# Kernel tuning notes

Measured on AMD Instinct MI355X. Metric: run time of the kernel, lower is better.

Reference implementation:

```python
import jax, jax.numpy as jnp
import numpy as np

N_ATOMS = 5000
N_EDGES = 100000
F = 128          # num_features
B = 20           # num_basis (sinc expansion)
L = 3            # num_interactions
CUTOFF = 5.0
NUM_EMB = 119


def setup_inputs() -> dict:
    key = jax.random.key(0)
    ks = jax.random.split(key, 16)
    Z = jax.random.randint(ks[0], (N_ATOMS,), 1, NUM_EMB)
    edge_idx = jax.random.randint(ks[1], (N_EDGES, 2), 0, N_ATOMS)
    edge_dist = jax.random.uniform(ks[2], (N_EDGES,), minval=0.5, maxval=6.0, dtype=jnp.float32)
    u = jax.random.normal(ks[3], (N_EDGES, 3), dtype=jnp.float32)
    u = u / jnp.linalg.norm(u, axis=-1, keepdims=True)
    edge_diff = u * edge_dist[:, None]  # displacement vectors with |d| == edge_dist
    s = lambda k, shape: (jax.random.normal(k, shape, dtype=jnp.float32) * 0.05)
    inp = dict(Z=Z, edge_idx=edge_idx, edge_diff=edge_diff, edge_dist=edge_dist)
    inp.update(
        emb=s(ks[4], (NUM_EMB, F)),
        msg_w1=s(ks[5], (L, F, F)), msg_b1=jnp.zeros((L, F), jnp.float32),
        msg_w2=s(ks[6], (L, F, 3 * F)), msg_b2=jnp.zeros((L, 3 * F), jnp.float32),
        filt_w=s(ks[7], (L, B, 3 * F)), filt_b=jnp.zeros((L, 3 * F), jnp.float32),
        upd_U=s(ks[8], (L, F, F)), upd_V=s(ks[9], (L, F, F)),
        upd_w1=s(ks[10], (L, 2 * F, F)), upd_b1=jnp.zeros((L, F), jnp.float32),
        upd_w2=s(ks[11], (L, F, 3 * F)), upd_b2=jnp.zeros((L, 3 * F), jnp.float32),
        ro_w1=s(ks[12], (F, F // 2)), ro_b1=jnp.zeros((F // 2,), jnp.float32),
        ro_w2=s(ks[13], (F // 2, 1)), ro_b2=jnp.zeros((1,), jnp.float32),
    )
    return inp


def _painn(Z, edge_idx, edge_diff, edge_dist,
           emb, msg_w1, msg_b1, msg_w2, msg_b2, filt_w, filt_b,
           upd_U, upd_V, upd_w1, upd_b1, upd_w2, upd_b2,
           ro_w1, ro_b1, ro_w2, ro_b2):
    dtype = edge_diff.dtype
    # edge mask (equivalent to boolean compaction: masked edges contribute 0)
    mask = (edge_dist < CUTOFF).astype(dtype)
    dst = edge_idx[:, 0]  # receiver (index_add target)
    src = edge_idx[:, 1]  # sender (gathered neighbor)
    # sinc radial expansion: sin(n*pi*r/rc)/r, n = 1..B
    n = jnp.arange(1, B + 1, dtype=dtype)
    rbf = jnp.sin(edge_dist[:, None] * n * (jnp.pi / CUTOFF)) / edge_dist[:, None]  # [E,B]
    # cosine cutoff envelope, zeroed outside cutoff
    fc = 0.5 * (jnp.cos(jnp.pi * edge_dist / CUTOFF) + 1.0)
    env = (fc * mask)[:, None]  # [E,1]
    unit = edge_diff / edge_dist[:, None]  # [E,3]

    s_feat = emb[Z]                                   # [N,F]
    v_feat = jnp.zeros((Z.shape[0], 3, F), dtype)     # [N,3,F]

    for l in range(L):
        # ---- PainnMessage ----
        filt = (rbf @ filt_w[l] + filt_b[l]) * env                           # [E,3F]
        phi = jax.nn.silu(s_feat @ msg_w1[l] + msg_b1[l]) @ msg_w2[l] + msg_b2[l]  # [N,3F]
        fo = filt * phi[src]                                                  # [E,3F]
        gsv, gev, ms = jnp.split(fo, 3, axis=-1)                              # each [E,F]
        mv = v_feat[src] * gsv[:, None, :] + gev[:, None, :] * unit[:, :, None]  # [E,3,F]
        s_feat = s_feat + jnp.zeros_like(s_feat).at[dst].add(ms)
        v_feat = v_feat + jnp.zeros_like(v_feat).at[dst].add(mv)
        # ---- PainnUpdate ----
        Uv = jnp.einsum('nif,fg->nig', v_feat, upd_U[l])   # [N,3,F]
        Vv = jnp.einsum('nif,fg->nig', v_feat, upd_V[l])   # [N,3,F]
        Vn = jnp.linalg.norm(Vv, axis=1)                   # [N,F]
        a = jax.nn.silu(jnp.concatenate([s_feat, Vn], axis=-1) @ upd_w1[l] + upd_b1[l]) @ upd_w2[l] + upd_b2[l]
        avv, asv, ass = jnp.split(a, 3, axis=-1)
        v_feat = v_feat + avv[:, None, :] * Uv
        s_feat = s_feat + asv * jnp.sum(Uv * Vv, axis=1) + ass

    # atomwise readout MLP -> per-atom energy
    atom_energy = (jax.nn.silu(s_feat @ ro_w1 + ro_b1) @ ro_w2 + ro_b2)[:, 0]  # [N]
    return atom_energy


def reference(Z, edge_idx, edge_diff, edge_dist,
              emb, msg_w1, msg_b1, msg_w2, msg_b2, filt_w, filt_b,
              upd_U, upd_V, upd_w1, upd_b1, upd_w2, upd_b2,
              ro_w1, ro_b1, ro_w2, ro_b2):
    return _painn(Z, edge_idx, edge_diff, edge_dist,
                  emb, msg_w1, msg_b1, msg_w2, msg_b2, filt_w, filt_b,
                  upd_U, upd_V, upd_w1, upd_b1, upd_w2, upd_b2,
                  ro_w1, ro_b1, ro_w2, ro_b2)
```

## Files before the change

kernel.cpp:

```cpp
#include <hip/hip_runtime.h>
#include <hip/hip_bf16.h>
#include <hip/hip_fp16.h>
#include <math.h>

#define N_ATOMS 5000
#define N_EDGES 100000
#define F 128
#define B 20
#define NL 3
#define CAP 64

constexpr float CUTOFF = 5.0f;
constexpr float PI_F = 3.14159265358979323846f;

typedef _Float16 f16x8 __attribute__((ext_vector_type(8)));
typedef _Float16 h2 __attribute__((ext_vector_type(2)));
typedef float f32x4 __attribute__((ext_vector_type(4)));

struct EMeta { int src; float env; float u0, u1, u2; int pad[3]; };
struct __align__(4) U3 { unsigned int x, y, z; };

__device__ __forceinline__ float silu_f(float x) { return x / (1.0f + __expf(-x)); }

#define PV_IDX(atom, t) (((size_t)(atom) * F + (t)) * 6)

__global__ void init_kernel(const int* __restrict__ Z, const float* __restrict__ emb,
                            float* __restrict__ s, _Float16* __restrict__ s_h,
                            float* __restrict__ v, _Float16* __restrict__ pv,
                            int* __restrict__ count) {
    int atom = blockIdx.x;
    int t = threadIdx.x;
    float val = emb[Z[atom] * F + t];
    s[atom * F + t] = val;
    s_h[atom * F + t] = (_Float16)val;
#pragma unroll
    for (int d = 0; d < 3; ++d) v[(size_t)atom * 3 * F + d * F + t] = 0.0f;
    unsigned int* pp = (unsigned int*)(pv + PV_IDX(atom, t));
    pp[0] = 0u; pp[1] = 0u; pp[2] = 0u;
    if (t == 0) count[atom] = 0;
}

__global__ void fill_buckets(const int* __restrict__ eidx, int* __restrict__ count,
                             int* __restrict__ bucket) {
    int e = blockIdx.x * 256 + threadIdx.x;
    if (e >= N_EDGES) return;
    int dst = eidx[2 * e];
    int pos = atomicAdd(&count[dst], 1);
    if (pos < CAP) bucket[dst * CAP + pos] = e;
}

__global__ void edge_meta_kernel(const int* __restrict__ count, const int* __restrict__ bucket,
                                 const int* __restrict__ eidx, const float* __restrict__ ediff,
                                 const float* __restrict__ edist,
                                 EMeta* __restrict__ meta, _Float16* __restrict__ rbfh) {
    int slot = blockIdx.x * 256 + threadIdx.x;
    if (slot >= N_ATOMS * CAP) return;
    int a = slot / CAP, i = slot % CAP;
    if (i >= count[a]) return;
    int e = bucket[slot];
    float d = edist[e];
    EMeta m;
    m.src = eidx[2 * e + 1];
    float fc = 0.5f * (cosf(PI_F * d / CUTOFF) + 1.0f);
    m.env = (d < CUTOFF) ? fc : 0.0f;
    float inv = 1.0f / d;
    m.u0 = ediff[3 * e + 0] * inv;
    m.u1 = ediff[3 * e + 1] * inv;
    m.u2 = ediff[3 * e + 2] * inv;
    m.pad[0] = m.pad[1] = m.pad[2] = 0;
    meta[slot] = m;
    _Float16* rp = rbfh + (size_t)slot * 24;
#pragma unroll
    for (int b = 0; b < B; ++b)
        rp[b] = (_Float16)(sinf(d * (float)(b + 1) * (PI_F / CUTOFF)) / d);
    rp[20] = rp[21] = rp[22] = rp[23] = (_Float16)0.0f;
}

struct TPlanX { const float* src; void* dst; int R, C, blk0, isf16, pad; };
struct TPlansX { TPlanX p[24]; int n; };

__global__ void transpose_x(TPlansX P) {
    int b = blockIdx.x;
    int pi = 0;
#pragma unroll
    for (int i = 1; i < 24; ++i)
        if (i < P.n && b >= P.p[i].blk0) pi = i;
    const float* src = P.p[pi].src;
    int R = P.p[pi].R, C = P.p[pi].C, pad = P.p[pi].pad;
    int f = (b - P.p[pi].blk0) * 256 + threadIdx.x;
    if (f < R * C) {
        int c = f / R, r = f - c * R;
        float val = src[r * C + c];
        if (P.p[pi].isf16) ((_Float16*)P.p[pi].dst)[c * pad + r] = (_Float16)val;
        else ((float*)P.p[pi].dst)[c * pad + r] = val;
    }
}

__global__ __launch_bounds__(256) void phi_mlp_kernel(
    const _Float16* __restrict__ s_h, const _Float16* __restrict__ w1T,
    const float* __restrict__ b1, const _Float16* __restrict__ w2T,
    const float* __restrict__ b2, _Float16* __restrict__ pv) {
    __shared__ __align__(16) _Float16 shA[16 * 136];
    __shared__ __align__(16) _Float16 shH[16 * 136];
    int r0 = blockIdx.x * 16;
    int tid = threadIdx.x;
    {
        int r = tid >> 4, c8 = (tid & 15) * 8;
        int rg = r0 + r; if (rg >= N_ATOMS) rg = N_ATOMS - 1;
        *(f16x8*)(shA + r * 136 + c8) = *(const f16x8*)(s_h + (size_t)rg * F + c8);
    }
    __syncthreads();
    int lane = tid & 63, wv = tid >> 6;
    int col = lane & 15, quad = lane >> 4;
    for (int nt = wv; nt < 8; nt += 4) {
        int n = nt * 16 + col;
        f32x4 acc = {0.f, 0.f, 0.f, 0.f};
#pragma unroll
        for (int kt = 0; kt < 4; ++kt) {
            f16x8 afr = *(const f16x8*)(shA + col * 136 + kt * 32 + quad * 8);
            f16x8 bfr = *(const f16x8*)(w1T + (size_t)n * 128 + kt * 32 + quad * 8);
            acc = __builtin_amdgcn_mfma_f32_16x16x32_f16(afr, bfr, acc, 0, 0, 0);
        }
        float bb = b1[n];
#pragma unroll
        for (int r = 0; r < 4; ++r)
            shH[(quad * 4 + r) * 136 + n] = (_Float16)silu_f(acc[r] + bb);
    }
    __syncthreads();
    for (int nt = wv; nt < 24; nt += 4) {
        int n = nt * 16 + col;
        f32x4 acc = {0.f, 0.f, 0.f, 0.f};
#pragma unroll
        for (int kt = 0; kt < 4; ++kt) {
            f16x8 afr = *(const f16x8*)(shH + col * 136 + kt * 32 + quad * 8);
            f16x8 bfr = *(const f16x8*)(w2T + (size_t)n * 128 + kt * 32 + quad * 8);
            acc = __builtin_amdgcn_mfma_f32_16x16x32_f16(afr, bfr, acc, 0, 0, 0);
        }
        float bb = b2[n];
#pragma unroll
        for (int r = 0; r < 4; ++r) {
            int row = r0 + quad * 4 + r;
            if (row < N_ATOMS)
                pv[PV_IDX(row, n & 127) + (n >> 7)] = (_Float16)(acc[r] + bb);
        }
    }
}

__global__ __launch_bounds__(256) void edge_agg_kernel(
    const int* __restrict__ count, const EMeta* __restrict__ meta,
    const _Float16* __restrict__ rbfh,
    const _Float16* __restrict__ fwT,
    const float* __restrict__ fb,
    const _Float16* __restrict__ pv,
    float* __restrict__ s, float* __restrict__ v,
    _Float16* __restrict__ vmid_h) {
    int a = blockIdx.x;
    int tid = threadIdx.x;
    int t = tid & 127;
    int team = tid >> 7;

    unsigned int rw0[10], rw1[10], rw2[10];
    {
        const unsigned int* p0 = (const unsigned int*)(fwT + (size_t)t * 24);
        const unsigned int* p1 = (const unsigned int*)(fwT + (size_t)(F + t) * 24);
        const unsigned int* p2 = (const unsigned int*)(fwT + (size_t)(2 * F + t) * 24);
#pragma unroll
        for (int j = 0; j < 10; ++j) { rw0[j] = p0[j]; rw1[j] = p1[j]; rw2[j] = p2[j]; }
    }
    float fb0 = fb[t], fb1 = fb[F + t], fb2 = fb[2 * F + t];

    int n = count[a]; if (n > CAP) n = CAP;
    float accS = 0.f, accV0 = 0.f, accV1 = 0.f, accV2 = 0.f;

    __shared__ int sh_src[32];
    __shared__ float sh_env[32];
    __shared__ float sh_unit[32][3];
    __shared__ __align__(16) unsigned int sh_rbf[32 * 12];
    __shared__ __align__(16) float sh_part[4][F];
    const size_t aC = (size_t)a * CAP;
    const unsigned int* rbf32 = (const unsigned int*)rbfh;

    for (int base = 0; base < n; base += 32) {
        int cnt = min(32, n - base);
        __syncthreads();
        if (tid < cnt) {
            EMeta m = meta[aC + base + tid];
            sh_src[tid] = m.src;
            sh_env[tid] = m.env;
            sh_unit[tid][0] = m.u0; sh_unit[tid][1] = m.u1; sh_unit[tid][2] = m.u2;
        }
        for (int task = tid; task < cnt * 12; task += 256) {
            int i = task / 12, w = task - i * 12;
            sh_rbf[i * 12 + w] = rbf32[(aC + base + i) * 12 + w];
        }
        __syncthreads();

        int myCnt = (cnt > team) ? ((cnt - team + 1) >> 1) : 0;
        if (myCnt > 0) {
            U3 QA[4], QB[4];
            int ngrp = (myCnt + 3) >> 2;

            auto load_grp = [&](int gbase, U3 Q[4]) {
#pragma unroll
                for (int j = 0; j < 4; ++j) {
                    int i = gbase + j;
                    int ii = (i < myCnt) ? i : (myCnt - 1);
                    int src = sh_src[team + 2 * ii];
                    Q[j] = *(const U3*)(pv + PV_IDX(src, t));
                }
            };
            auto comp_grp = [&](int gbase, U3 Q[4]) {
#pragma unroll
                for (int j = 0; j < 4; ++j) {
                    int i = gbase + j;
                    if (i < myCnt) {
                        int ei = team + 2 * i;
                        const uint4* rq = (const uint4*)(sh_rbf + ei * 12);
                        uint4 qa = rq[0], qb = rq[1];
                        uint2 qc = *(const uint2*)(sh_rbf + ei * 12 + 8);
                        unsigned int rr[10] = {qa.x, qa.y, qa.z, qa.w,
                                               qb.x, qb.y, qb.z, qb.w, qc.x, qc.y};
                        float f0 = fb0, f1 = fb1, f2 = fb2;
#pragma unroll
                        for (int p = 0; p < 10; ++p) {
                            h2 rb = __builtin_bit_cast(h2, rr[p]);
                            f0 = __builtin_amdgcn_fdot2(rb, __builtin_bit_cast(h2, rw0[p]), f0, false);
                            f1 = __builtin_amdgcn_fdot2(rb, __builtin_bit_cast(h2, rw1[p]), f1, false);
                            f2 = __builtin_amdgcn_fdot2(rb, __builtin_bit_cast(h2, rw2[p]), f2, false);
                        }
                        float env = sh_env[ei];
                        f0 *= env; f1 *= env; f2 *= env;
                        h2 q0 = __builtin_bit_cast(h2, Q[j].x);
                        h2 q1 = __builtin_bit_cast(h2, Q[j].y);
                        h2 q2 = __builtin_bit_cast(h2, Q[j].z);
                        accS += f2 * (float)q1[0];
                        float gsv = f0 * (float)q0[0];
                        float gev = f1 * (float)q0[1];
                        accV0 += (float)q1[1] * gsv + gev * sh_unit[ei][0];
                        accV1 += (float)q2[0] * gsv + gev * sh_unit[ei][1];
                        accV2 += (float)q2[1] * gsv + gev * sh_unit[ei][2];
                    }
                }
            };

            load_grp(0, QA);
            for (int g = 0; g < ngrp; g += 2) {
                if (g + 1 < ngrp) load_grp((g + 1) * 4, QB);
                comp_grp(g * 4, QA);
                if (g + 1 < ngrp) {
                    if (g + 2 < ngrp) load_grp((g + 2) * 4, QA);
                    comp_grp((g + 1) * 4, QB);
                }
            }
        }
    }

    __syncthreads();
    if (team == 1) {
        sh_part[0][t] = accS; sh_part[1][t] = accV0;
        sh_part[2][t] = accV1; sh_part[3][t] = accV2;
    }
    __syncthreads();
    if (team == 0) {
        float sm = s[a * F + t] + accS + sh_part[0][t];
        s[a * F + t] = sm;
        float vm0 = v[a * 3 * F + t] + accV0 + sh_part[1][t];
        float vm1 = v[a * 3 * F + F + t] + accV1 + sh_part[2][t];
        float vm2 = v[a * 3 * F + 2 * F + t] + accV2 + sh_part[3][t];
        v[a * 3 * F + t] = vm0;
        v[a * 3 * F + F + t] = vm1;
        v[a * 3 * F + 2 * F + t] = vm2;
        vmid_h[(size_t)(a * 3 + 0) * F + t] = (_Float16)vm0;
        vmid_h[(size_t)(a * 3 + 1) * F + t] = (_Float16)vm1;
        vmid_h[(size_t)(a * 3 + 2) * F + t] = (_Float16)vm2;
    }
}

__global__ __launch_bounds__(512) void fused_update_kernel(
    const _Float16* __restrict__ vmid_h, const _Float16* __restrict__ uvT,
    const _Float16* __restrict__ w1T, const float* __restrict__ b1,
    const _Float16* __restrict__ w2T, const float* __restrict__ b2,
    float* __restrict__ s, float* __restrict__ v, _Float16* __restrict__ pv,
    const _Float16* __restrict__ nw1T, const float* __restrict__ nb1,
    const _Float16* __restrict__ nw2T, const float* __restrict__ nb2,
    int do_phi,
    const _Float16* __restrict__ roT16, const float* __restrict__ rb1,
    const float* __restrict__ rw2, const float* __restrict__ rb2,
    float* __restrict__ out, int do_ro) {
    __shared__ __align__(16) _Float16 shA[48 * 136];
    __shared__ __align__(16) _Float16 shUV[48 * 264];
    __shared__ __align__(16) _Float16 shCat[16 * 264];
    __shared__ __align__(16) _Float16 shH[16 * 136];
    __shared__ __align__(16) _Float16 shAa[16 * 392];
    _Float16* shS = shA;
    float* shRO = (float*)shAa;
    int a0 = blockIdx.x * 16;
    int r0 = a0 * 3;
    int tid = threadIdx.x;
    for (int slot = tid; slot < 48 * 16; slot += 512) {
        int r = slot >> 4, c8 = (slot & 15) * 8;
        int rg = r0 + r; if (rg >= N_ATOMS * 3) rg = N_ATOMS * 3 - 1;
        *(f16x8*)(shA + r * 136 + c8) = *(const f16x8*)(vmid_h + (size_t)rg * F + c8);
    }
    __syncthreads();
    int lane = tid & 63, wv = tid >> 6;
    int col = lane & 15, quad = lane >> 4;

    for (int j = wv; j < 48; j += 8) {
        int mt = j >> 4, nt = j & 15;
        int n = nt * 16 + col;
        f32x4 acc = {0.f, 0.f, 0.f, 0.f};
#pragma unroll
        for (int kt = 0; kt < 4; ++kt) {
            f16x8 afr = *(const f16x8*)(shA + (mt * 16 + col) * 136 + kt * 32 + quad * 8);
            f16x8 bfr = *(const f16x8*)(uvT + (size_t)n * 128 + kt * 32 + quad * 8);
            acc = __builtin_amdgcn_mfma_f32_16x16x32_f16(afr, bfr, acc, 0, 0, 0);
        }
#pragma unroll
        for (int r = 0; r < 4; ++r)
            shUV[(mt * 16 + quad * 4 + r) * 264 + n] = (_Float16)acc[r];
    }
    __syncthreads();

    for (int p = tid; p < 2048; p += 512) {
        int ai = p >> 7, t = p & 127;
        int atom = a0 + ai;
        int ag = (atom < N_ATOMS) ? atom : N_ATOMS - 1;
        shCat[ai * 264 + t] = (_Float16)s[(size_t)ag * F + t];
        float x0 = (float)shUV[(ai * 3 + 0) * 264 + 128 + t];
        float x1 = (float)shUV[(ai * 3 + 1) * 264 + 128 + t];
        float x2 = (float)shUV[(ai * 3 + 2) * 264 + 128 + t];
        shCat[ai * 264 + 128 + t] = (_Float16)sqrtf(x0 * x0 + x1 * x1 + x2 * x2);
    }
    __syncthreads();

    for (int nt = wv; nt < 8; nt += 8) {
        int n = nt * 16 + col;
        f32x4 acc = {0.f, 0.f, 0.f, 0.f};
#pragma unroll
        for (int kt = 0; kt < 8; ++kt) {
            f16x8 afr = *(const f16x8*)(shCat + col * 264 + kt * 32 + quad * 8);
            f16x8 bfr = *(const f16x8*)(w1T + (size_t)n * 256 + kt * 32 + quad * 8);
            acc = __builtin_amdgcn_mfma_f32_16x16x32_f16(afr, bfr, acc, 0, 0, 0);
        }
        float bb = b1[n];
#pragma unroll
        for (int r = 0; r < 4; ++r)
            shH[(quad * 4 + r) * 136 + n] = (_Float16)silu_f(acc[r] + bb);
    }
    __syncthreads();

    for (int nt = wv; nt < 24; nt += 8) {
        int n = nt * 16 + col;
        f32x4 acc = {0.f, 0.f, 0.f, 0.f};
#pragma unroll
        for (int kt = 0; kt < 4; ++kt) {
            f16x8 afr = *(const f16x8*)(shH + col * 136 + kt * 32 + quad * 8);
            f16x8 bfr = *(const f16x8*)(w2T + (size_t)n * 128 + kt * 32 + quad * 8);
            acc = __builtin_amdgcn_mfma_f32_16x16x32_f16(afr, bfr, acc, 0, 0, 0);
        }
        float bb = b2[n];
#pragma unroll
        for (int r = 0; r < 4; ++r)
            shAa[(quad * 4 + r) * 392 + n] = (_Float16)(acc[r] + bb);
    }
    __syncthreads();

    for (int p = tid; p < 2048; p += 512) {
        int ai = p >> 7, t = p & 127;
        int atom = a0 + ai;
        if (atom >= N_ATOMS) { shS[ai * 136 + t] = (_Float16)0.0f; continue; }
        float avv = (float)shAa[ai * 392 + t];
        float asv = (float)shAa[ai * 392 + 128 + t];
        float ass = (float)shAa[ai * 392 + 256 + t];
        float dot = 0.f;
        _Float16* pvp = pv + PV_IDX(atom, t);
#pragma unroll
        for (int d = 0; d < 3; ++d) {
            float u = (float)shUV[(ai * 3 + d) * 264 + t];
            float w = (float)shUV[(ai * 3 + d) * 264 + 128 + t];
            dot += u * w;
            float nv = v[(size_t)atom * 3 * F + d * F + t] + avv * u;
            v[(size_t)atom * 3 * F + d * F + t] = nv;
            pvp[3 + d] = (_Float16)nv;
        }
        float sn = s[(size_t)atom * F + t] + asv * dot + ass;
        s[(size_t)atom * F + t] = sn;
        shS[ai * 136 + t] = (_Float16)sn;
    }

    if (do_phi) {
        __syncthreads();
        for (int nt = wv; nt < 8; nt += 8) {
            int n = nt * 16 + col;
            f32x4 acc = {0.f, 0.f, 0.f, 0.f};
#pragma unroll
            for (int kt = 0; kt < 4; ++kt) {
                f16x8 afr = *(const f16x8*)(shS + col * 136 + kt * 32 + quad * 8);
                f16x8 bfr = *(const f16x8*)(nw1T + (size_t)n * 128 + kt * 32 + quad * 8);
                acc = __builtin_amdgcn_mfma_f32_16x16x32_f16(afr, bfr, acc, 0, 0, 0);
            }
            float bb = nb1[n];
#pragma unroll
            for (int r = 0; r < 4; ++r)
                shH[(quad * 4 + r) * 136 + n] = (_Float16)silu_f(acc[r] + bb);
        }
        __syncthreads();
        for (int nt = wv; nt < 24; nt += 8) {
            int n = nt * 16 + col;
            f32x4 acc = {0.f, 0.f, 0.f, 0.f};
#pragma unroll
            for (int kt = 0; kt < 4; ++kt) {
                f16x8 afr = *(const f16x8*)(shH + col * 136 + kt * 32 + quad * 8);
                f16x8 bfr = *(const f16x8*)(nw2T + (size_t)n * 128 + kt * 32 + quad * 8);
                acc = __builtin_amdgcn_mfma_f32_16x16x32_f16(afr, bfr, acc, 0, 0, 0);
            }
            float bb = nb2[n];
#pragma unroll
            for (int r = 0; r < 4; ++r) {
                int row = a0 + quad * 4 + r;
                if (row < N_ATOMS)
                    pv[PV_IDX(row, n & 127) + (n >> 7)] = (_Float16)(acc[r] + bb);
            }
        }
    }

    if (do_ro) {
        __syncthreads();
        if (wv < 4) {
            int n = wv * 16 + col;
            f32x4 acc = {0.f, 0.f, 0.f, 0.f};
#pragma unroll
            for (int kt = 0; kt < 4; ++kt) {
                f16x8 afr = *(const f16x8*)(shS + col * 136 + kt * 32 + quad * 8);
                f16x8 bfr = *(const f16x8*)(roT16 + (size_t)n * 128 + kt * 32 + quad * 8);
                acc = __builtin_amdgcn_mfma_f32_16x16x32_f16(afr, bfr, acc, 0, 0, 0);
            }
            float bb = rb1[n], w2n = rw2[n];
#pragma unroll
            for (int r = 0; r < 4; ++r)
                shRO[(quad * 4 + r) * 68 + n] = silu_f(acc[r] + bb) * w2n;
        }
        __syncthreads();
        if (tid < 16) {
            int atom = a0 + tid;
            if (atom < N_ATOMS) {
                float sum = rb2[0];
#pragma unroll 8
                for (int k = 0; k < 64; ++k) sum += shRO[tid * 68 + k];
                out[atom] = sum;
            }
        }
    }
}

extern "C" void kernel_launch(void* const* d_in, const int* in_sizes, int n_in,
                              void* d_out, int out_size, void* d_ws, size_t ws_size,
                              hipStream_t stream) {
    const int*   Z      = (const int*)d_in[0];
    const int*   eidx   = (const int*)d_in[1];
    const float* ediff  = (const float*)d_in[2];
    const float* edist  = (const float*)d_in[3];
    const float* emb    = (const float*)d_in[4];
    const float* msg_w1 = (const float*)d_in[5];
    const float* msg_b1 = (const float*)d_in[6];
    const float* msg_w2 = (const float*)d_in[7];
    const float* msg_b2 = (const float*)d_in[8];
    const float* filt_w = (const float*)d_in[9];
    const float* filt_b = (const float*)d_in[10];
    const float* upd_U  = (const float*)d_in[11];
    const float* upd_V  = (const float*)d_in[12];
    const float* upd_w1 = (const float*)d_in[13];
    const float* upd_b1 = (const float*)d_in[14];
    const float* upd_w2 = (const float*)d_in[15];
    const float* upd_b2 = (const float*)d_in[16];
    const float* ro_w1  = (const float*)d_in[17];
    const float* ro_b1  = (const float*)d_in[18];
    const float* ro_w2  = (const float*)d_in[19];
    const float* ro_b2  = (const float*)d_in[20];
    float* out = (float*)d_out;

    float* ws = (float*)d_ws;
    float* s   = ws;
    float* v   = s + N_ATOMS * F;
    int* count  = (int*)(v + N_ATOMS * 3 * F);
    int* bucket = count + N_ATOMS;
    EMeta* meta = (EMeta*)(bucket + N_ATOMS * CAP);
    _Float16* rbfh = (_Float16*)(meta + N_ATOMS * CAP);
    _Float16* s_h    = rbfh + (size_t)N_ATOMS * CAP * 24;
    _Float16* vmid_h = s_h + (size_t)N_ATOMS * F;
    _Float16* pv     = vmid_h + (size_t)N_ATOMS * 3 * F;
    _Float16* wh     = pv + (size_t)N_ATOMS * F * 6;

    const int HWL = 16384 + 49152 + 32768 + 32768 + 49152 + 384 * 24;
    _Float16* mw1T = wh;
    _Float16* mw2T = wh + 16384;
    _Float16* uvT  = wh + 65536;
    _Float16* uw1T = wh + 98304;
    _Float16* uw2T = wh + 131072;
    _Float16* fwTl = wh + 180224;
    _Float16* roT16 = wh + (size_t)NL * HWL;

    TPlansX P; int nb = 0, pi = 0;
    auto add = [&](const float* src, void* dst, int R, int C, int isf16, int pad) {
        P.p[pi].src = src; P.p[pi].dst = dst; P.p[pi].R = R; P.p[pi].C = C;
        P.p[pi].blk0 = nb; P.p[pi].isf16 = isf16; P.p[pi].pad = pad;
        nb += (R * C + 255) / 256; ++pi;
    };
    for (int l = 0; l < NL; ++l) {
        add(msg_w1 + l * F * F,     mw1T + (size_t)l * HWL, F, F, 1, F);
        add(msg_w2 + l * F * 3 * F, mw2T + (size_t)l * HWL, F, 3 * F, 1, F);
        add(upd_U  + l * F * F,     uvT  + (size_t)l * HWL, F, F, 1, F);
        add(upd_V  + l * F * F,     uvT  + (size_t)l * HWL + F * F, F, F, 1, F);
        add(upd_w1 + l * 2 * F * F, uw1T + (size_t)l * HWL, 2 * F, F, 1, 2 * F);
        add(upd_w2 + l * F * 3 * F, uw2T + (size_t)l * HWL, F, 3 * F, 1, F);
        add(filt_w + l * B * 3 * F, fwTl + (size_t)l * HWL, B, 3 * F, 1, 24);
    }
    add(ro_w1, roT16, F, 64, 1, F);
    P.n = pi;

    init_kernel<<<N_ATOMS, F, 0, stream>>>(Z, emb, s, s_h, v, pv, count);
    fill_buckets<<<(N_EDGES + 255) / 256, 256, 0, stream>>>(eidx, count, bucket);
    transpose_x<<<nb, 256, 0, stream>>>(P);
    edge_meta_kernel<<<(N_ATOMS * CAP + 255) / 256, 256, 0, stream>>>(
        count, bucket, eidx, ediff, edist, meta, rbfh);

    const int GB16 = (N_ATOMS + 15) / 16;
    phi_mlp_kernel<<<GB16, 256, 0, stream>>>(
        s_h, mw1T, msg_b1, mw2T, msg_b2, pv);
    for (int l = 0; l < NL; ++l) {
        edge_agg_kernel<<<N_ATOMS, 256, 0, stream>>>(
            count, meta, rbfh, fwTl + (size_t)l * HWL, filt_b + l * 3 * F,
            pv, s, v, vmid_h);
        int do_phi = (l + 1 < NL);
        int do_ro = (l == NL - 1);
        int ln = do_phi ? (l + 1) : l;
        fused_update_kernel<<<GB16, 512, 0, stream>>>(
            vmid_h, uvT + (size_t)l * HWL,
            uw1T + (size_t)l * HWL, upd_b1 + l * F,
            uw2T + (size_t)l * HWL, upd_b2 + l * 3 * F,
            s, v, pv,
            mw1T + (size_t)ln * HWL, msg_b1 + ln * F,
            mw2T + (size_t)ln * HWL, msg_b2 + ln * 3 * F, do_phi,
            roT16, ro_b1, ro_w2, ro_b2, out, do_ro);
    }
}
```

Before: 359.3 us.

## Merge preprocessing launches, tile weight transposes, and single-pass edge aggregation

Folds atom init, bucket filling and weight transposition into one prep kernel, and edge-meta computation plus the first message MLP into a second, which cuts launch count. The count array is now cleared with a memset instead. The weight transpose now goes through a 32x32 shared-memory tile so both reads and writes are coalesced. The sinc basis is built with a Chebyshev sine recurrence from one __sinf/__cosf pair instead of 20 sinf calls, which adds small approximation error. The aggregation kernel stages all up to 64 neighbours at once to drop the per-32 loop and barriers, and the pv message buffer is double-buffered across layers.

```diff
diff --git a/kernel.cpp b/kernel.cpp
--- a/kernel.cpp
+++ b/kernel.cpp
@@ -24,86 +24,111 @@
 
 #define PV_IDX(atom, t) (((size_t)(atom) * F + (t)) * 6)
 
-__global__ void init_kernel(const int* __restrict__ Z, const float* __restrict__ emb,
-                            float* __restrict__ s, _Float16* __restrict__ s_h,
-                            float* __restrict__ v, _Float16* __restrict__ pv,
-                            int* __restrict__ count) {
-    int atom = blockIdx.x;
-    int t = threadIdx.x;
-    float val = emb[Z[atom] * F + t];
-    s[atom * F + t] = val;
-    s_h[atom * F + t] = (_Float16)val;
-#pragma unroll
-    for (int d = 0; d < 3; ++d) v[(size_t)atom * 3 * F + d * F + t] = 0.0f;
-    unsigned int* pp = (unsigned int*)(pv + PV_IDX(atom, t));
-    pp[0] = 0u; pp[1] = 0u; pp[2] = 0u;
-    if (t == 0) count[atom] = 0;
+#define NB_INIT 2500
+#define NB_BUCK 391
+
+struct TPlanT { const float* src; _Float16* dst; int R, C, pad, blk0, tpc; };
+struct TPlansT { TPlanT p[22]; int n; };
+
+__global__ __launch_bounds__(256) void prep_kernel(
+    const int* __restrict__ Z, const float* __restrict__ emb,
+    float* __restrict__ s, _Float16* __restrict__ s_h,
+    float* __restrict__ v, _Float16* __restrict__ pv,
+    const int* __restrict__ eidx, int* __restrict__ count, int* __restrict__ bucket,
+    TPlansT P) {
+    __shared__ float tile[32][33];
+    int b = blockIdx.x, tid = threadIdx.x;
+    if (b < NB_INIT) {
+        int atom = b * 2 + (tid >> 7);
+        int t = tid & 127;
+        float val = emb[Z[atom] * F + t];
+        s[(size_t)atom * F + t] = val;
+        s_h[(size_t)atom * F + t] = (_Float16)val;
+#pragma unroll
+        for (int d = 0; d < 3; ++d) v[((size_t)atom * 3 + d) * F + t] = 0.0f;
+        unsigned int* pp = (unsigned int*)(pv + PV_IDX(atom, t));
+        pp[0] = 0u; pp[1] = 0u; pp[2] = 0u;
+        return;
+    }
+    if (b < NB_INIT + NB_BUCK) {
+        int e = (b - NB_INIT) * 256 + tid;
+        if (e < N_EDGES) {
+            int dst = eidx[2 * e];
+            int pos = atomicAdd(&count[dst], 1);
+            if (pos < CAP) bucket[dst * CAP + pos] = e;
+        }
+        return;
+    }
+    int tb = b - (NB_INIT + NB_BUCK);
+    int pi = 0;
+#pragma unroll
+    for (int i = 1; i < 22; ++i)
+        if (i < P.n && tb >= P.p[i].blk0) pi = i;
+    const float* src = P.p[pi].src;
+    _Float16* dst = P.p[pi].dst;
+    int R = P.p[pi].R, C = P.p[pi].C, pad = P.p[pi].pad;
+    int tl = tb - P.p[pi].blk0;
+    int tpc = P.p[pi].tpc;
+    int tr0 = (tl / tpc) * 32, tc0 = (tl % tpc) * 32;
+    int i = tid >> 5, j = tid & 31;
+#pragma unroll
+    for (int rr = 0; rr < 4; ++rr) {
+        int r = tr0 + i + 8 * rr, c = tc0 + j;
+        if (r < R && c < C) tile[i + 8 * rr][j] = src[(size_t)r * C + c];
+    }
+    __syncthreads();
+#pragma unroll
+    for (int rr = 0; rr < 4; ++rr) {
+        int c = tc0 + i + 8 * rr, r = tr0 + j;
+        if (c < C && r < R) dst[(size_t)c * pad + r] = (_Float16)tile[j][i + 8 * rr];
+    }
 }
 
-__global__ void fill_buckets(const int* __restrict__ eidx, int* __restrict__ count,
-                             int* __restrict__ bucket) {
-    int e = blockIdx.x * 256 + threadIdx.x;
-    if (e >= N_EDGES) return;
-    int dst = eidx[2 * e];
-    int pos = atomicAdd(&count[dst], 1);
-    if (pos < CAP) bucket[dst * CAP + pos] = e;
-}
-
-__global__ void edge_meta_kernel(const int* __restrict__ count, const int* __restrict__ bucket,
-                                 const int* __restrict__ eidx, const float* __restrict__ ediff,
-                                 const float* __restrict__ edist,
-                                 EMeta* __restrict__ meta, _Float16* __restrict__ rbfh) {
-    int slot = blockIdx.x * 256 + threadIdx.x;
-    if (slot >= N_ATOMS * CAP) return;
-    int a = slot / CAP, i = slot % CAP;
-    if (i >= count[a]) return;
-    int e = bucket[slot];
-    float d = edist[e];
-    EMeta m;
-    m.src = eidx[2 * e + 1];
-    float fc = 0.5f * (cosf(PI_F * d / CUTOFF) + 1.0f);
-    m.env = (d < CUTOFF) ? fc : 0.0f;
-    float inv = 1.0f / d;
-    m.u0 = ediff[3 * e + 0] * inv;
-    m.u1 = ediff[3 * e + 1] * inv;
-    m.u2 = ediff[3 * e + 2] * inv;
-    m.pad[0] = m.pad[1] = m.pad[2] = 0;
-    meta[slot] = m;
-    _Float16* rp = rbfh + (size_t)slot * 24;
-#pragma unroll
-    for (int b = 0; b < B; ++b)
-        rp[b] = (_Float16)(sinf(d * (float)(b + 1) * (PI_F / CUTOFF)) / d);
-    rp[20] = rp[21] = rp[22] = rp[23] = (_Float16)0.0f;
-}
-
-struct TPlanX { const float* src; void* dst; int R, C, blk0, isf16, pad; };
-struct TPlansX { TPlanX p[24]; int n; };
-
-__global__ void transpose_x(TPlansX P) {
-    int b = blockIdx.x;
-    int pi = 0;
-#pragma unroll
-    for (int i = 1; i < 24; ++i)
-        if (i < P.n && b >= P.p[i].blk0) pi = i;
-    const float* src = P.p[pi].src;
-    int R = P.p[pi].R, C = P.p[pi].C, pad = P.p[pi].pad;
-    int f = (b - P.p[pi].blk0) * 256 + threadIdx.x;
-    if (f < R * C) {
-        int c = f / R, r = f - c * R;
-        float val = src[r * C + c];
-        if (P.p[pi].isf16) ((_Float16*)P.p[pi].dst)[c * pad + r] = (_Float16)val;
-        else ((float*)P.p[pi].dst)[c * pad + r] = val;
-    }
-}
-
-__global__ __launch_bounds__(256) void phi_mlp_kernel(
+#define NB_META 1250
+
+__global__ __launch_bounds__(256) void meta_phi_kernel(
+    const int* __restrict__ count, const int* __restrict__ bucket,
+    const int* __restrict__ eidx, const float* __restrict__ ediff,
+    const float* __restrict__ edist,
+    EMeta* __restrict__ meta, _Float16* __restrict__ rbfh,
     const _Float16* __restrict__ s_h, const _Float16* __restrict__ w1T,
     const float* __restrict__ b1, const _Float16* __restrict__ w2T,
     const float* __restrict__ b2, _Float16* __restrict__ pv) {
     __shared__ __align__(16) _Float16 shA[16 * 136];
     __shared__ __align__(16) _Float16 shH[16 * 136];
-    int r0 = blockIdx.x * 16;
-    int tid = threadIdx.x;
+    int b = blockIdx.x, tid = threadIdx.x;
+    if (b < NB_META) {
+        int slot = b * 256 + tid;
+        int a = slot >> 6, i = slot & (CAP - 1);
+        if (i >= count[a]) return;
+        int e = bucket[slot];
+        float d = edist[e];
+        EMeta m;
+        m.src = eidx[2 * e + 1];
+        float theta = d * (PI_F / CUTOFF);
+        float s1 = __sinf(theta), c1 = __cosf(theta);
+        float fc = 0.5f * (c1 + 1.0f);
+        m.env = (d < CUTOFF) ? fc : 0.0f;
+        float inv = 1.0f / d;
+        m.u0 = ediff[3 * e + 0] * inv;
+        m.u1 = ediff[3 * e + 1] * inv;
+        m.u2 = ediff[3 * e + 2] * inv;
+        m.pad[0] = m.pad[1] = m.pad[2] = 0;
+        meta[slot] = m;
+        _Float16* rp = rbfh + (size_t)slot * 24;
+        float twoc = 2.0f * c1;
+        float skm2 = 0.0f, skm1 = s1;
+        rp[0] = (_Float16)(s1 * inv);
+#pragma unroll
+        for (int k = 2; k <= B; ++k) {
+            float sk = twoc * skm1 - skm2;
+            skm2 = skm1; skm1 = sk;
+            rp[k - 1] = (_Float16)(sk * inv);
+        }
+        rp[20] = rp[21] = rp[22] = rp[23] = (_Float16)0.0f;
+        return;
+    }
+    int r0 = (b - NB_META) * 16;
     {
         int r = tid >> 4, c8 = (tid & 15) * 8;
         int rg = r0 + r; if (rg >= N_ATOMS) rg = N_ATOMS - 1;
@@ -146,130 +171,120 @@
     }
 }
 
-__global__ __launch_bounds__(256) void edge_agg_kernel(
+__global__ __launch_bounds__(256) void agg_kernel(
     const int* __restrict__ count, const EMeta* __restrict__ meta,
     const _Float16* __restrict__ rbfh,
-    const _Float16* __restrict__ fwT,
-    const float* __restrict__ fb,
-    const _Float16* __restrict__ pv,
+    const _Float16* __restrict__ fwT, const float* __restrict__ fb,
+    const _Float16* __restrict__ pv_r,
     float* __restrict__ s, float* __restrict__ v,
     _Float16* __restrict__ vmid_h) {
     int a = blockIdx.x;
     int tid = threadIdx.x;
-    int t = tid & 127;
-    int team = tid >> 7;
-
-    unsigned int rw0[10], rw1[10], rw2[10];
+    int t = tid & 127, team = tid >> 7;
+
+    unsigned int frw0[10], frw1[10], frw2[10];
     {
         const unsigned int* p0 = (const unsigned int*)(fwT + (size_t)t * 24);
         const unsigned int* p1 = (const unsigned int*)(fwT + (size_t)(F + t) * 24);
         const unsigned int* p2 = (const unsigned int*)(fwT + (size_t)(2 * F + t) * 24);
 #pragma unroll
-        for (int j = 0; j < 10; ++j) { rw0[j] = p0[j]; rw1[j] = p1[j]; rw2[j] = p2[j]; }
+        for (int j = 0; j < 10; ++j) { frw0[j] = p0[j]; frw1[j] = p1[j]; frw2[j] = p2[j]; }
     }
     float fb0 = fb[t], fb1 = fb[F + t], fb2 = fb[2 * F + t];
 
+    __shared__ int sh_src[CAP];
+    __shared__ float sh_env[CAP];
+    __shared__ float sh_unit[CAP][3];
+    __shared__ __align__(16) unsigned int sh_rbf[CAP * 12];
+    __shared__ float sh_part[4][F];
+
     int n = count[a]; if (n > CAP) n = CAP;
+    const size_t aC = (size_t)a * CAP;
+    if (tid < n) {
+        EMeta m = meta[aC + tid];
+        sh_src[tid] = m.src;
+        sh_env[tid] = m.env;
+        sh_unit[tid][0] = m.u0; sh_unit[tid][1] = m.u1; sh_unit[tid][2] = m.u2;
+    }
+    const unsigned int* rbf32 = (const unsigned int*)rbfh;
+    for (int task = tid; task < n * 12; task += 256) {
+        int i = task / 12, w = task - i * 12;
+        sh_rbf[i * 12 + w] = rbf32[(aC + i) * 12 + w];
+    }
+    __syncthreads();
+
     float accS = 0.f, accV0 = 0.f, accV1 = 0.f, accV2 = 0.f;
-
-    __shared__ int sh_src[32];
-    __shared__ float sh_env[32];
-    __shared__ float sh_unit[32][3];
-    __shared__ __align__(16) unsigned int sh_rbf[32 * 12];
-    __shared__ __align__(16) float sh_part[4][F];
-    const size_t aC = (size_t)a * CAP;
-    const unsigned int* rbf32 = (const unsigned int*)rbfh;
-
-    for (int base = 0; base < n; base += 32) {
-        int cnt = min(32, n - base);
-        __syncthreads();
-        if (tid < cnt) {
-            EMeta m = meta[aC + base + tid];
-            sh_src[tid] = m.src;
-            sh_env[tid] = m.env;
-            sh_unit[tid][0] = m.u0; sh_unit[tid][1] = m.u1; sh_unit[tid][2] = m.u2;
-        }
-        for (int task = tid; task < cnt * 12; task += 256) {
-            int i = task / 12, w = task - i * 12;
-            sh_rbf[i * 12 + w] = rbf32[(aC + base + i) * 12 + w];
-        }
-        __syncthreads();
-
-        int myCnt = (cnt > team) ? ((cnt - team + 1) >> 1) : 0;
-        if (myCnt > 0) {
-            U3 QA[4], QB[4];
-            int ngrp = (myCnt + 3) >> 2;
-
-            auto load_grp = [&](int gbase, U3 Q[4]) {
-#pragma unroll
-                for (int j = 0; j < 4; ++j) {
-                    int i = gbase + j;
-                    int ii = (i < myCnt) ? i : (myCnt - 1);
-                    int src = sh_src[team + 2 * ii];
-                    Q[j] = *(const U3*)(pv + PV_IDX(src, t));
+    int myCnt = (n > team) ? ((n - team + 1) >> 1) : 0;
+    if (myCnt > 0) {
+        U3 QA[4], QB[4];
+        int ngrp = (myCnt + 3) >> 2;
+        auto load_grp = [&](int gbase, U3 Q[4]) {
+#pragma unroll
+            for (int j = 0; j < 4; ++j) {
+                int i = gbase + j;
+                int ii = (i < myCnt) ? i : (myCnt - 1);
+                int src = sh_src[team + 2 * ii];
+                Q[j] = *(const U3*)(pv_r + PV_IDX(src, t));
+            }
+        };
+        auto comp_grp = [&](int gbase, U3 Q[4]) {
+#pragma unroll
+            for (int j = 0; j < 4; ++j) {
+                int i = gbase + j;
+                if (i < myCnt) {
+                    int ei = team + 2 * i;
+                    const uint4* rq = (const uint4*)(sh_rbf + ei * 12);
+                    uint4 qa = rq[0], qb = rq[1];
+                    uint2 qc = *(const uint2*)(sh_rbf + ei * 12 + 8);
+                    unsigned int rr[10] = {qa.x, qa.y, qa.z, qa.w,
+                                           qb.x, qb.y, qb.z, qb.w, qc.x, qc.y};
+                    float f0 = fb0, f1 = fb1, f2 = fb2;
+#pragma unroll
+                    for (int p = 0; p < 10; ++p) {
+                        h2 rb = __builtin_bit_cast(h2, rr[p]);
+                        f0 = __builtin_amdgcn_fdot2(rb, __builtin_bit_cast(h2, frw0[p]), f0, false);
+                        f1 = __builtin_amdgcn_fdot2(rb, __builtin_bit_cast(h2, frw1[p]), f1, false);
+                        f2 = __builtin_amdgcn_fdot2(rb, __builtin_bit_cast(h2, frw2[p]), f2, false);
+                    }
+                    float env = sh_env[ei];
+                    f0 *= env; f1 *= env; f2 *= env;
+                    h2 q0 = __builtin_bit_cast(h2, Q[j].x);
+                    h2 q1 = __builtin_bit_cast(h2, Q[j].y);
+                    h2 q2 = __builtin_bit_cast(h2, Q[j].z);
+                    accS += f2 * (float)q1[0];
+                    float gsv = f0 * (float)q0[0];
+                    float gev = f1 * (float)q0[1];
+                    accV0 += (float)q1[1] * gsv + gev * sh_unit[ei][0];
+                    accV1 += (float)q2[0] * gsv + gev * sh_unit[ei][1];
+                    accV2 += (float)q2[1] * gsv + gev * sh_unit[ei][2];
                 }
-            };
-            auto comp_grp = [&](int gbase, U3 Q[4]) {
-#pragma unroll
-                for (int j = 0; j < 4; ++j) {
-                    int i = gbase + j;
-                    if (i < myCnt) {
-                        int ei = team + 2 * i;
-                        const uint4* rq = (const uint4*)(sh_rbf + ei * 12);
-                        uint4 qa = rq[0], qb = rq[1];
-                        uint2 qc = *(const uint2*)(sh_rbf + ei * 12 + 8);
-                        unsigned int rr[10] = {qa.x, qa.y, qa.z, qa.w,
-                                               qb.x, qb.y, qb.z, qb.w, qc.x, qc.y};
-                        float f0 = fb0, f1 = fb1, f2 = fb2;
-#pragma unroll
-                        for (int p = 0; p < 10; ++p) {
-                            h2 rb = __builtin_bit_cast(h2, rr[p]);
-                            f0 = __builtin_amdgcn_fdot2(rb, __builtin_bit_cast(h2, rw0[p]), f0, false);
-                            f1 = __builtin_amdgcn_fdot2(rb, __builtin_bit_cast(h2, rw1[p]), f1, false);
-                            f2 = __builtin_amdgcn_fdot2(rb, __builtin_bit_cast(h2, rw2[p]), f2, false);
-                        }
-                        float env = sh_env[ei];
-                        f0 *= env; f1 *= env; f2 *= env;
-                        h2 q0 = __builtin_bit_cast(h2, Q[j].x);
-                        h2 q1 = __builtin_bit_cast(h2, Q[j].y);
-                        h2 q2 = __builtin_bit_cast(h2, Q[j].z);
-                        accS += f2 * (float)q1[0];
-                        float gsv = f0 * (float)q0[0];
-                        float gev = f1 * (float)q0[1];
-                        accV0 += (float)q1[1] * gsv + gev * sh_unit[ei][0];
-                        accV1 += (float)q2[0] * gsv + gev * sh_unit[ei][1];
-                        accV2 += (float)q2[1] * gsv + gev * sh_unit[ei][2];
-                    }
-                }
-            };
-
-            load_grp(0, QA);
-            for (int g = 0; g < ngrp; g += 2) {
-                if (g + 1 < ngrp) load_grp((g + 1) * 4, QB);
-                comp_grp(g * 4, QA);
-                if (g + 1 < ngrp) {
-                    if (g + 2 < ngrp) load_grp((g + 2) * 4, QA);
-                    comp_grp((g + 1) * 4, QB);
-                }
-            }
-        }
-    }
-
-    __syncthreads();
+            }
+        };
+        load_grp(0, QA);
+        for (int g = 0; g < ngrp; g += 2) {
+            if (g + 1 < ngrp) load_grp((g + 1) * 4, QB);
+            comp_grp(g * 4, QA);
+            if (g + 1 < ngrp) {
+                if (g + 2 < ngrp) load_grp((g + 2) * 4, QA);
+                comp_grp((g + 1) * 4, QB);
+            }
+        }
+    }
+
     if (team == 1) {
         sh_part[0][t] = accS; sh_part[1][t] = accV0;
         sh_part[2][t] = accV1; sh_part[3][t] = accV2;
     }
     __syncthreads();
     if (team == 0) {
-        float sm = s[a * F + t] + accS + sh_part[0][t];
-        s[a * F + t] = sm;
-        float vm0 = v[a * 3 * F + t] + accV0 + sh_part[1][t];
-        float vm1 = v[a * 3 * F + F + t] + accV1 + sh_part[2][t];
-        float vm2 = v[a * 3 * F + 2 * F + t] + accV2 + sh_part[3][t];
-        v[a * 3 * F + t] = vm0;
-        v[a * 3 * F + F + t] = vm1;
-        v[a * 3 * F + 2 * F + t] = vm2;
+        float sm = s[(size_t)a * F + t] + accS + sh_part[0][t];
+        s[(size_t)a * F + t] = sm;
+        float vm0 = v[(size_t)a * 3 * F + t] + accV0 + sh_part[1][t];
+        float vm1 = v[(size_t)a * 3 * F + F + t] + accV1 + sh_part[2][t];
+        float vm2 = v[(size_t)a * 3 * F + 2 * F + t] + accV2 + sh_part[3][t];
+        v[(size_t)a * 3 * F + t] = vm0;
+        v[(size_t)a * 3 * F + F + t] = vm1;
+        v[(size_t)a * 3 * F + 2 * F + t] = vm2;
         vmid_h[(size_t)(a * 3 + 0) * F + t] = (_Float16)vm0;
         vmid_h[(size_t)(a * 3 + 1) * F + t] = (_Float16)vm1;
         vmid_h[(size_t)(a * 3 + 2) * F + t] = (_Float16)vm2;
@@ -280,12 +295,12 @@
     const _Float16* __restrict__ vmid_h, const _Float16* __restrict__ uvT,
     const _Float16* __restrict__ w1T, const float* __restrict__ b1,
     const _Float16* __restrict__ w2T, const float* __restrict__ b2,
-    float* __restrict__ s, float* __restrict__ v, _Float16* __restrict__ pv,
+    float* __restrict__ s, float* __restrict__ v, _Float16* __restrict__ pv_w,
     const _Float16* __restrict__ nw1T, const float* __restrict__ nb1,
     const _Float16* __restrict__ nw2T, const float* __restrict__ nb2,
     int do_phi,
     const _Float16* __restrict__ roT16, const float* __restrict__ rb1,
-    const float* __restrict__ rw2, const float* __restrict__ rb2,
+    const float* __restrict__ ro_w2p, const float* __restrict__ rb2,
     float* __restrict__ out, int do_ro) {
     __shared__ __align__(16) _Float16 shA[48 * 136];
     __shared__ __align__(16) _Float16 shUV[48 * 264];
@@ -374,7 +389,7 @@
         float asv = (float)shAa[ai * 392 + 128 + t];
         float ass = (float)shAa[ai * 392 + 256 + t];
         float dot = 0.f;
-        _Float16* pvp = pv + PV_IDX(atom, t);
+        _Float16* pvp = pv_w + PV_IDX(atom, t);
 #pragma unroll
         for (int d = 0; d < 3; ++d) {
             float u = (float)shUV[(ai * 3 + d) * 264 + t];
@@ -420,7 +435,7 @@
             for (int r = 0; r < 4; ++r) {
                 int row = a0 + quad * 4 + r;
                 if (row < N_ATOMS)
-                    pv[PV_IDX(row, n & 127) + (n >> 7)] = (_Float16)(acc[r] + bb);
+                    pv_w[PV_IDX(row, n & 127) + (n >> 7)] = (_Float16)(acc[r] + bb);
             }
         }
     }
@@ -436,7 +451,7 @@
                 f16x8 bfr = *(const f16x8*)(roT16 + (size_t)n * 128 + kt * 32 + quad * 8);
                 acc = __builtin_amdgcn_mfma_f32_16x16x32_f16(afr, bfr, acc, 0, 0, 0);
             }
-            float bb = rb1[n], w2n = rw2[n];
+            float bb = rb1[n], w2n = ro_w2p[n];
 #pragma unroll
             for (int r = 0; r < 4; ++r)
                 shRO[(quad * 4 + r) * 68 + n] = silu_f(acc[r] + bb) * w2n;
@@ -487,10 +502,11 @@
     int* bucket = count + N_ATOMS;
     EMeta* meta = (EMeta*)(bucket + N_ATOMS * CAP);
     _Float16* rbfh = (_Float16*)(meta + N_ATOMS * CAP);
-    _Float16* s_h    = rbfh + (size_t)N_ATOMS * CAP * 24;
+    _Float16* s_h  = rbfh + (size_t)N_ATOMS * CAP * 24;
     _Float16* vmid_h = s_h + (size_t)N_ATOMS * F;
-    _Float16* pv     = vmid_h + (size_t)N_ATOMS * 3 * F;
-    _Float16* wh     = pv + (size_t)N_ATOMS * F * 6;
+    _Float16* pvA  = vmid_h + (size_t)N_ATOMS * 3 * F;
+    _Float16* pvB  = pvA + (size_t)N_ATOMS * F * 6;
+    _Float16* wh   = pvB + (size_t)N_ATOMS * F * 6;
 
     const int HWL = 16384 + 49152 + 32768 + 32768 + 49152 + 384 * 24;
     _Float16* mw1T = wh;
@@ -501,47 +517,54 @@
     _Float16* fwTl = wh + 180224;
     _Float16* roT16 = wh + (size_t)NL * HWL;
 
-    TPlansX P; int nb = 0, pi = 0;
-    auto add = [&](const float* src, void* dst, int R, int C, int isf16, int pad) {
-        P.p[pi].src = src; P.p[pi].dst = dst; P.p[pi].R = R; P.p[pi].C = C;
-        P.p[pi].blk0 = nb; P.p[pi].isf16 = isf16; P.p[pi].pad = pad;
-        nb += (R * C + 255) / 256; ++pi;
+    TPlansT P; int nb = 0, pi = 0;
+    auto add = [&](const float* src, _Float16* dst, int R, int C, int pad) {
+        int tr = (R + 31) / 32, tc = (C + 31) / 32;
+        P.p[pi].src = src; P.p[pi].dst = dst;
+        P.p[pi].R = R; P.p[pi].C = C; P.p[pi].pad = pad;
+        P.p[pi].blk0 = nb; P.p[pi].tpc = tc;
+        nb += tr * tc; ++pi;
     };
     for (int l = 0; l < NL; ++l) {
-        add(msg_w1 + l * F * F,     mw1T + (size_t)l * HWL, F, F, 1, F);
-        add(msg_w2 + l * F * 3 * F, mw2T + (size_t)l * HWL, F, 3 * F, 1, F);
-        add(upd_U  + l * F * F,     uvT  + (size_t)l * HWL, F, F, 1, F);
-        add(upd_V  + l * F * F,     uvT  + (size_t)l * HWL + F * F, F, F, 1, F);
-        add(upd_w1 + l * 2 * F * F, uw1T + (size_t)l * HWL, 2 * F, F, 1, 2 * F);
-        add(upd_w2 + l * F * 3 * F, uw2T + (size_t)l * HWL, F, 3 * F, 1, F);
-        add(filt_w + l * B * 3 * F, fwTl + (size_t)l * HWL, B, 3 * F, 1, 24);
-    }
-    add(ro_w1, roT16, F, 64, 1, F);
+        add(msg_w1 + l * F * F,     mw1T + (size_t)l * HWL, F, F, F);
+        add(msg_w2 + l * F * 3 * F, mw2T + (size_t)l * HWL, F, 3 * F, F);
+        add(upd_U  + l * F * F,     uvT  + (size_t)l * HWL, F, F, F);
+        add(upd_V  + l * F * F,     uvT  + (size_t)l * HWL + F * F, F, F, F);
+        add(upd_w1 + l * 2 * F * F, uw1T + (size_t)l * HWL, 2 * F, F, 2 * F);
+        add(upd_w2 + l * F * 3 * F, uw2T + (size_t)l * HWL, F, 3 * F, F);
+        add(filt_w + l * B * 3 * F, fwTl + (size_t)l * HWL, B, 3 * F, 24);
+    }
+    add(ro_w1, roT16, F, 64, F);
     P.n = pi;
 
-    init_kernel<<<N_ATOMS, F, 0, stream>>>(Z, emb, s, s_h, v, pv, count);
-    fill_buckets<<<(N_EDGES + 255) / 256, 256, 0, stream>>>(eidx, count, bucket);
-    transpose_x<<<nb, 256, 0, stream>>>(P);
-    edge_meta_kernel<<<(N_ATOMS * CAP + 255) / 256, 256, 0, stream>>>(
-        count, bucket, eidx, ediff, edist, meta, rbfh);
+    (void)hipMemsetAsync(count, 0, N_ATOMS * sizeof(int), stream);
+
+    prep_kernel<<<NB_INIT + NB_BUCK + nb, 256, 0, stream>>>(
+        Z, emb, s, s_h, v, pvA, eidx, count, bucket, P);
 
     const int GB16 = (N_ATOMS + 15) / 16;
-    phi_mlp_kernel<<<GB16, 256, 0, stream>>>(
-        s_h, mw1T, msg_b1, mw2T, msg_b2, pv);
+    meta_phi_kernel<<<NB_META + GB16, 256, 0, stream>>>(
+        count, bucket, eidx, ediff, edist, meta, rbfh,
+        s_h, mw1T, msg_b1, mw2T, msg_b2, pvA);
+
+    _Float16* pr = pvA;
+    _Float16* pw = pvB;
     for (int l = 0; l < NL; ++l) {
-        edge_agg_kernel<<<N_ATOMS, 256, 0, stream>>>(
-            count, meta, rbfh, fwTl + (size_t)l * HWL, filt_b + l * 3 * F,
-            pv, s, v, vmid_h);
         int do_phi = (l + 1 < NL);
         int do_ro = (l == NL - 1);
         int ln = do_phi ? (l + 1) : l;
+        agg_kernel<<<N_ATOMS, 256, 0, stream>>>(
+            count, meta, rbfh,
+            fwTl + (size_t)l * HWL, filt_b + l * 3 * F,
+            pr, s, v, vmid_h);
         fused_update_kernel<<<GB16, 512, 0, stream>>>(
             vmid_h, uvT + (size_t)l * HWL,
             uw1T + (size_t)l * HWL, upd_b1 + l * F,
             uw2T + (size_t)l * HWL, upd_b2 + l * 3 * F,
-            s, v, pv,
+            s, v, pw,
             mw1T + (size_t)ln * HWL, msg_b1 + ln * F,
             mw2T + (size_t)ln * HWL, msg_b2 + ln * 3 * F, do_phi,
             roT16, ro_b1, ro_w2, ro_b2, out, do_ro);
+        _Float16* tmp = pr; pr = pw; pw = tmp;
     }
 }
```

New measurement: 325.6 us. 1.1x faster.
